# Performance work log

Hardware: AMD Instinct MI355X
Metric: run time of the kernel (lower is better)

## Reference

```python
import jax, jax.numpy as jnp
import numpy as np

B, L, H, V = 64, 2048, 256, 32000
BETA = 0.9
EPS_K = 1e-6   # delta-rule key-norm eps (matches torch 1e-06)
EPS_LN = 1e-5  # torch LayerNorm default eps


def setup_inputs() -> dict:
    key = jax.random.key(0)
    ks = jax.random.split(key, 8)
    s = lambda k, shape: (jax.random.normal(k, shape, jnp.float32) * 0.02)
    return {
        "seq": jax.random.randint(ks[0], (B, L), 0, V),
        "embed": s(ks[1], (V, H)),
        "W1": s(ks[2], (H, 2 * H)),
        "b1": jnp.zeros((2 * H,), jnp.float32),
        "W2": s(ks[3], (2 * H, H)),
        "b2": jnp.zeros((H,), jnp.float32),
        "gamma": jnp.ones((H,), jnp.float32),
        "beta_ln": jnp.zeros((H,), jnp.float32),
        "rp_W": s(ks[4], (H, H)),
        "rp_b": jnp.zeros((H,), jnp.float32),
        "out_W": s(ks[5], (H, V)),
        "out_b": jnp.zeros((V,), jnp.float32),
    }


def reference(seq, embed, W1, b1, W2, b2, gamma, beta_ln, rp_W, rp_b, out_W, out_b):
    # Encoder: embed -> FFN residual -> LayerNorm
    e = embed[seq]                                    # [B, L, H]
    ff = jnp.maximum(e @ W1 + b1, 0.0) @ W2 + b2      # [B, L, H]
    x = e + ff
    mu = jnp.mean(x, axis=-1, keepdims=True)
    var = jnp.mean((x - mu) ** 2, axis=-1, keepdims=True)
    h_all = (x - mu) / jnp.sqrt(var + EPS_LN) * gamma + beta_ln  # [B, L, H]

    # Momentum delta-rule fast-weight memory over first L-1 steps (k == v == h_t)
    ks_t = jnp.moveaxis(h_all[:, :-1, :], 1, 0)       # [L-1, B, H] time-major

    def step(M, k):
        vp = jnp.einsum('bij,bj->bi', M, k)            # predicted value
        d = k - vp / (jnp.sum(k * k, axis=-1, keepdims=True) + EPS_K)
        delta = d[:, :, None] * k[:, None, :]          # outer product [B, H, H]
        return BETA * M + (1.0 - BETA) * delta, None

    M0 = jnp.zeros((h_all.shape[0], H, H), h_all.dtype)
    M, _ = jax.lax.scan(step, M0, ks_t)

    # Readout with final token
    y = jnp.einsum('bij,bj->bi', M, h_all[:, -1, :])   # [B, H]
    return (y @ rp_W + rp_b) @ out_W + out_b           # [B, V]
```

## Files before the change

kernel.cpp:

```cpp
#include <hip/hip_runtime.h>


#define B_ 64
#define L_ 2048
#define H_ 256
#define V_ 32000

typedef unsigned short u16;
typedef __attribute__((ext_vector_type(8))) short bf16x8;
typedef __attribute__((ext_vector_type(16))) float f32x16;
typedef __attribute__((ext_vector_type(4))) float f32x4;

__device__ __forceinline__ float b2f(u16 u){ union{unsigned x; float f;} z; z.x = ((unsigned)u)<<16; return z.f; }
__device__ __forceinline__ u16 f2b(float f){ union{float f; unsigned x;} z; z.f = f; unsigned r = z.x + 0x7FFFu + ((z.x>>16)&1u); return (u16)(r>>16); }
__device__ __forceinline__ float san(float v){ return (v == v && v > -1e30f && v < 1e30f) ? v : 0.f; }

template<bool F32> __device__ __forceinline__ float ldw(const void* p, long i){
  if (F32) return ((const float*)p)[i];
  return b2f(((const u16*)p)[i]);
}
template<bool F32> __device__ __forceinline__ float4 ld4(const void* p, long i){
  if (F32) return *(const float4*)((const float*)p + i);
  ushort4 u = *(const ushort4*)((const u16*)p + i);
  return make_float4(b2f(u.x), b2f(u.y), b2f(u.z), b2f(u.w));
}

__device__ __forceinline__ int detect_f32(const void* embed){
  const u16* e = (const u16*)embed;
  unsigned v = e[2 * (threadIdx.x & 255)];
  int ex = (v >> 7) & 0xFF;
  int pl = (ex >= 0x66 && ex <= 0x7D) || ((v & 0x7FFFu) == 0u);
  int cnt = __syncthreads_count(pl);
  return cnt < 128;
}

__global__ __launch_bounds__(256) void sentinel_kernel(const void* embed, void* out, float val)
{
  int f32 = detect_f32(embed);
  long idx = (long)blockIdx.x * 256 + threadIdx.x;
  if (idx < (long)B_ * V_){
    if (f32) ((float*)out)[idx] = val;
    else     ((u16*)out)[idx]   = f2b(val);
  }
}

template<bool F32>
__device__ __forceinline__ void wprep_body(
    const void* __restrict__ W1, const void* __restrict__ W2,
    u16* __restrict__ w1f_hi, u16* __restrict__ w1f_lo,
    u16* __restrict__ w2f_hi, u16* __restrict__ w2f_lo)
{
  const int cid = blockIdx.x * 256 + threadIdx.x;
  const int lane = cid & 63;
  const int nl = lane & 31, kh = lane >> 5;
  if (cid < 16384){
    const int nt = cid >> 10, k16 = (cid >> 6) & 15;
    const int n = nt*32 + nl;
    const int k0 = k16*16 + kh*8;
    #pragma unroll
    for (int e = 0; e < 8; ++e){
      float v = ldw<F32>(W1, (long)(k0+e)*512 + n);
      unsigned bi = __float_as_uint(v);
      u16 hi = (u16)(bi >> 16);
      float hif = __uint_as_float(((unsigned)hi) << 16);
      w1f_hi[cid*8 + e] = hi;
      w1f_lo[cid*8 + e] = f2b(v - hif);
    }
  } else {
    const int c2 = cid - 16384;
    const int nt = c2 >> 11, k16 = (c2 >> 6) & 31;
    const int n = nt*32 + nl;
    const int k0 = k16*16 + kh*8;
    #pragma unroll
    for (int e = 0; e < 8; ++e){
      float v = ldw<F32>(W2, (long)(k0+e)*256 + n);
      unsigned bi = __float_as_uint(v);
      u16 hi = (u16)(bi >> 16);
      float hif = __uint_as_float(((unsigned)hi) << 16);
      w2f_hi[c2*8 + e] = hi;
      w2f_lo[c2*8 + e] = f2b(v - hif);
    }
  }
}

__global__ __launch_bounds__(256) void wprep_kernel(
    const void* __restrict__ embed,
    const void* __restrict__ W1, const void* __restrict__ W2,
    u16* __restrict__ wbuf)
{
  u16* w1h = wbuf;
  u16* w1l = wbuf + 131072;
  u16* w2h = wbuf + 262144;
  u16* w2l = wbuf + 393216;
  if (detect_f32(embed)) wprep_body<true >(W1, W2, w1h, w1l, w2h, w2l);
  else                   wprep_body<false>(W1, W2, w1h, w1l, w2h, w2l);
}

template<bool F32>
__device__ __forceinline__ void encm_body(
    u16* e_l, u16* t1_l, float* red, float* red2, float* stats,
    const int* __restrict__ seq, const void* __restrict__ embed,
    const u16* __restrict__ w1f_hi, const u16* __restrict__ w1f_lo,
    const u16* __restrict__ w2f_hi, const u16* __restrict__ w2f_lo,
    const void* __restrict__ b1, const void* __restrict__ b2,
    const void* __restrict__ gamma, const void* __restrict__ beta,
    u16* __restrict__ h)
{
  const int tid = threadIdx.x;
  const long tok0 = (long)blockIdx.x * 32;
  const int lane = tid & 63, wv = tid >> 6;
  const int col = lane & 31, hw = lane >> 5;

  {
    const int tr = tid >> 3, u0 = (tid & 7) * 4;
    int tk = seq[tok0 + tr];
    tk = (tk >= 0 && tk < V_) ? tk : 0;
    #pragma unroll
    for (int c = 0; c < 4; ++c){
      const int u = u0 + c;
      const int phys = u ^ (tr & 7);
      if (F32){
        const float4* sp = (const float4*)((const float*)embed + (long)tk*H_ + u*8);
        float4 v0 = sp[0], v1 = sp[1];
        ushort4 o0, o1;
        o0.x=f2b(v0.x); o0.y=f2b(v0.y); o0.z=f2b(v0.z); o0.w=f2b(v0.w);
        o1.x=f2b(v1.x); o1.y=f2b(v1.y); o1.z=f2b(v1.z); o1.w=f2b(v1.w);
        *(ushort4*)&e_l[tr*256 + phys*8]     = o0;
        *(ushort4*)&e_l[tr*256 + phys*8 + 4] = o1;
      } else {
        uint4 v = *(const uint4*)((const u16*)embed + (long)tk*H_ + u*8);
        *(uint4*)&e_l[tr*256 + phys*8] = v;
      }
    }
  }
  __syncthreads();

  {
    f32x16 acc[4];
    #pragma unroll
    for (int t = 0; t < 4; ++t)
      #pragma unroll
      for (int r = 0; r < 16; ++r) acc[t][r] = 0.f;

    #pragma unroll
    for (int k16 = 0; k16 < 16; ++k16){
      const int phys = (k16*2 + hw) ^ (col & 7);
      bf16x8 a = *(const bf16x8*)&e_l[col*256 + phys*8];
      #pragma unroll
      for (int t = 0; t < 4; ++t){
        const int off = (((wv*4 + t)*16 + k16)*64 + lane)*8;
        bf16x8 bh = *(const bf16x8*)&w1f_hi[off];
        bf16x8 bl = *(const bf16x8*)&w1f_lo[off];
        acc[t] = __builtin_amdgcn_mfma_f32_32x32x16_bf16(a, bh, acc[t], 0, 0, 0);
        acc[t] = __builtin_amdgcn_mfma_f32_32x32x16_bf16(a, bl, acc[t], 0, 0, 0);
      }
    }

    #pragma unroll
    for (int t = 0; t < 4; ++t){
      const int n = (wv*4 + t)*32 + col;
      const float bb = ldw<F32>(b1, n);
      const int u = n >> 3, nl = n & 7;
      #pragma unroll
      for (int r = 0; r < 16; ++r){
        const int m = (r&3) + 8*(r>>2) + 4*hw;
        float v = fmaxf(acc[t][r] + bb, 0.f);
        t1_l[m*512 + ((u ^ (m&7))<<3) + nl] = f2b(v);
      }
    }
  }
  __syncthreads();

  f32x16 acc2[2];
  #pragma unroll
  for (int t = 0; t < 2; ++t)
    #pragma unroll
    for (int r = 0; r < 16; ++r) acc2[t][r] = 0.f;

  #pragma unroll
  for (int k16 = 0; k16 < 32; ++k16){
    const int phys = (k16*2 + hw) ^ (col & 7);
    bf16x8 a = *(const bf16x8*)&t1_l[col*512 + phys*8];
    #pragma unroll
    for (int t = 0; t < 2; ++t){
      const int off = (((wv*2 + t)*32 + k16)*64 + lane)*8;
      bf16x8 bh = *(const bf16x8*)&w2f_hi[off];
      bf16x8 bl = *(const bf16x8*)&w2f_lo[off];
      acc2[t] = __builtin_amdgcn_mfma_f32_32x32x16_bf16(a, bh, acc2[t], 0, 0, 0);
      acc2[t] = __builtin_amdgcn_mfma_f32_32x32x16_bf16(a, bl, acc2[t], 0, 0, 0);
    }
  }
  __syncthreads();

  u16* xb = t1_l;
  #pragma unroll
  for (int t = 0; t < 2; ++t){
    const int n = (wv*2 + t)*32 + col;
    const float bb = ldw<F32>(b2, n);
    const int ue = n >> 3, nl = n & 7;
    #pragma unroll
    for (int r = 0; r < 16; ++r){
      const int m = (r&3) + 8*(r>>2) + 4*hw;
      float ev = b2f(e_l[m*256 + ((ue ^ (m&7))<<3) + nl]);
      float x = acc2[t][r] + bb + ev;
      xb[m*256 + n] = f2b(x);
    }
  }
  __syncthreads();

  {
    const int row = tid >> 3, seg = tid & 7;
    const u16* xr = &xb[row*256 + seg*32];
    float s = 0.f, q = 0.f;
    #pragma unroll
    for (int j = 0; j < 32; j += 4){
      ushort4 v4 = *(const ushort4*)&xr[j];
      float v0 = b2f(v4.x), v1 = b2f(v4.y), v2 = b2f(v4.z), v3 = b2f(v4.w);
      s += v0 + v1 + v2 + v3;
      q += v0*v0 + v1*v1 + v2*v2 + v3*v3;
    }
    red[row*8 + seg] = s;
    red2[row*8 + seg] = q;
  }
  __syncthreads();
  if (tid < 32){
    float s = 0.f, q = 0.f;
    #pragma unroll
    for (int j = 0; j < 8; ++j){ s += red[tid*8 + j]; q += red2[tid*8 + j]; }
    float mu = s * (1.f/256.f);
    float var = q * (1.f/256.f) - mu*mu;
    stats[tid] = mu;
    stats[32 + tid] = 1.f / sqrtf(fmaxf(var, 0.f) + 1e-5f);
  }
  __syncthreads();

  {
    const int row = tid >> 3, c0 = (tid & 7) * 32;
    const float mu = stats[row], rs = stats[32 + row];
    u16* hp = h + (tok0 + row)*H_ + c0;
    const u16* xr = &xb[row*256 + c0];
    #pragma unroll
    for (int j = 0; j < 32; j += 4){
      float4 g  = ld4<F32>(gamma, c0 + j);
      float4 be = ld4<F32>(beta,  c0 + j);
      ushort4 xv = *(const ushort4*)&xr[j];
      ushort4 o;
      o.x = f2b(san((b2f(xv.x) - mu)*rs*g.x + be.x));
      o.y = f2b(san((b2f(xv.y) - mu)*rs*g.y + be.y));
      o.z = f2b(san((b2f(xv.z) - mu)*rs*g.z + be.z));
      o.w = f2b(san((b2f(xv.w) - mu)*rs*g.w + be.w));
      *(ushort4*)&hp[j] = o;
    }
  }
}

__global__ __launch_bounds__(256) void encm_kernel(
    const int* __restrict__ seq, const void* __restrict__ embed,
    const u16* __restrict__ wbuf,
    const void* __restrict__ b1, const void* __restrict__ b2,
    const void* __restrict__ gamma, const void* __restrict__ beta,
    u16* __restrict__ h)
{
  __shared__ __align__(16) u16 e_l[32*256];
  __shared__ __align__(16) u16 t1_l[32*512];
  __shared__ float red[256];
  __shared__ float red2[256];
  __shared__ float stats[64];
  const u16* w1h = wbuf;
  const u16* w1l = wbuf + 131072;
  const u16* w2h = wbuf + 262144;
  const u16* w2l = wbuf + 393216;
  if (detect_f32(embed))
    encm_body<true >(e_l, t1_l, red, red2, stats, seq, embed, w1h, w1l, w2h, w2l, b1, b2, gamma, beta, h);
  else
    encm_body<false>(e_l, t1_l, red, red2, stats, seq, embed, w1h, w1l, w2h, w2l, b1, b2, gamma, beta, h);
}

template<bool F32>
__device__ __forceinline__ void enc_body(
    u16* sm,
    const int* __restrict__ seq, const void* __restrict__ embed,
    const void* __restrict__ W1, const void* __restrict__ b1,
    const void* __restrict__ W2, const void* __restrict__ b2,
    const void* __restrict__ gamma, const void* __restrict__ beta,
    u16* __restrict__ h)
{
  u16* eT  = sm;
  u16* t1T = sm + 8192;
  u16* xb  = sm + 24576;
  float* stats = (float*)sm;

  const int tid = threadIdx.x;
  const long tok0 = (long)blockIdx.x * 32;

  for (int idx = tid; idx < 8192; idx += 256){
    int r = idx >> 8, c = idx & 255;
    int tk = seq[tok0 + r];
    tk = (tk >= 0 && tk < V_) ? tk : 0;
    eT[c*32 + r] = f2b(ldw<F32>(embed, (long)tk*H_ + c));
  }
  __syncthreads();

  const int jg = tid & 31, rg = tid >> 5;
  const int r0 = rg * 4;

  for (int sl = 0; sl < 4; ++sl){
    const int j0 = sl*128 + jg*4;
    float acc[4][4] = {{0.f}};
    for (int c = 0; c < 256; ++c){
      ushort4 a4 = *(const ushort4*)&eT[c*32 + r0];
      float4 w = ld4<F32>(W1, (long)c*512 + j0);
      float a0=b2f(a4.x), a1=b2f(a4.y), a2=b2f(a4.z), a3=b2f(a4.w);
      acc[0][0]+=a0*w.x; acc[0][1]+=a0*w.y; acc[0][2]+=a0*w.z; acc[0][3]+=a0*w.w;
      acc[1][0]+=a1*w.x; acc[1][1]+=a1*w.y; acc[1][2]+=a1*w.z; acc[1][3]+=a1*w.w;
      acc[2][0]+=a2*w.x; acc[2][1]+=a2*w.y; acc[2][2]+=a2*w.z; acc[2][3]+=a2*w.w;
      acc[3][0]+=a3*w.x; acc[3][1]+=a3*w.y; acc[3][2]+=a3*w.z; acc[3][3]+=a3*w.w;
    }
    for (int jj = 0; jj < 4; ++jj){
      float bb = ldw<F32>(b1, j0+jj);
      ushort4 o;
      o.x = f2b(fmaxf(acc[0][jj]+bb, 0.f));
      o.y = f2b(fmaxf(acc[1][jj]+bb, 0.f));
      o.z = f2b(fmaxf(acc[2][jj]+bb, 0.f));
      o.w = f2b(fmaxf(acc[3][jj]+bb, 0.f));
      *(ushort4*)&t1T[(j0+jj)*32 + r0] = o;
    }
  }
  __syncthreads();

  for (int sl = 0; sl < 2; ++sl){
    const int co0 = sl*128 + jg*4;
    float acc[4][4] = {{0.f}};
    for (int c = 0; c < 512; ++c){
      ushort4 a4 = *(const ushort4*)&t1T[c*32 + r0];
      float4 w = ld4<F32>(W2, (long)c*256 + co0);
      float a0=b2f(a4.x), a1=b2f(a4.y), a2=b2f(a4.z), a3=b2f(a4.w);
      acc[0][0]+=a0*w.x; acc[0][1]+=a0*w.y; acc[0][2]+=a0*w.z; acc[0][3]+=a0*w.w;
      acc[1][0]+=a1*w.x; acc[1][1]+=a1*w.y; acc[1][2]+=a1*w.z; acc[1][3]+=a1*w.w;
      acc[2][0]+=a2*w.x; acc[2][1]+=a2*w.y; acc[2][2]+=a2*w.z; acc[2][3]+=a2*w.w;
      acc[3][0]+=a3*w.x; acc[3][1]+=a3*w.y; acc[3][2]+=a3*w.z; acc[3][3]+=a3*w.w;
    }
    float bb0 = ldw<F32>(b2, co0+0), bb1 = ldw<F32>(b2, co0+1);
    float bb2 = ldw<F32>(b2, co0+2), bb3 = ldw<F32>(b2, co0+3);
    for (int rr = 0; rr < 4; ++rr){
      float x0 = acc[rr][0] + bb0 + b2f(eT[(co0+0)*32 + r0+rr]);
      float x1 = acc[rr][1] + bb1 + b2f(eT[(co0+1)*32 + r0+rr]);
      float x2 = acc[rr][2] + bb2 + b2f(eT[(co0+2)*32 + r0+rr]);
      float x3 = acc[rr][3] + bb3 + b2f(eT[(co0+3)*32 + r0+rr]);
      ushort4 o; o.x=f2b(x0); o.y=f2b(x1); o.z=f2b(x2); o.w=f2b(x3);
      *(ushort4*)&xb[(r0+rr)*256 + co0] = o;
    }
  }
  __syncthreads();

  if (tid < 32){
    float s = 0.f, q = 0.f;
    for (int c = 0; c < 256; ++c){ float v = b2f(xb[tid*256 + c]); s += v; q += v*v; }
    float mu = s * (1.f/256.f);
    float var = q * (1.f/256.f) - mu*mu;
    stats[tid] = mu;
    stats[32 + tid] = 1.f / sqrtf(fmaxf(var, 0.f) + 1e-5f);
  }
  __syncthreads();
  for (int idx = tid; idx < 8192; idx += 256){
    int r = idx >> 8, c = idx & 255;
    float hv = (b2f(xb[idx]) - stats[r]) * stats[32+r] * ldw<F32>(gamma, c) + ldw<F32>(beta, c);
    h[(tok0 + r)*H_ + c] = f2b(san(hv));
  }
}

__global__ __launch_bounds__(256) void enc_kernel(
    const int* __restrict__ seq, const void* __restrict__ embed,
    const void* __restrict__ W1, const void* __restrict__ b1,
    const void* __restrict__ W2, const void* __restrict__ b2,
    const void* __restrict__ gamma, const void* __restrict__ beta,
    u16* __restrict__ h)
{
  __shared__ __align__(16) u16 sm[32768];
  if (detect_f32(embed)) enc_body<true >(sm, seq, embed, W1, b1, W2, b2, gamma, beta, h);
  else                   enc_body<false>(sm, seq, embed, W1, b1, W2, b2, gamma, beta, h);
}

__global__ __launch_bounds__(64) void winv_kernel(
    const u16* __restrict__ h, u16* __restrict__ w2g, float* __restrict__ scg)
{
  __shared__ __align__(16) u16 k_l[32*256];
  __shared__ float g_l[32*33];
  __shared__ float w_l[32*33];
  __shared__ float bp[33];

  const int tid = threadIdx.x;
  const int cb = blockIdx.x;
  const int b = cb >> 6, ch = cb & 63;
  const int col = tid & 31, hw = tid >> 5;
  const int C = (ch == 63) ? 31 : 32;

  if (tid < 33) bp[tid] = powf(0.9f, (float)tid);

  {
    const int t = tid >> 1, u0 = (tid & 1) * 16;
    const u16* src = h + ((long)b*L_ + ch*32 + t)*H_ + u0*8;
    #pragma unroll
    for (int c = 0; c < 16; ++c){
      uint4 v = make_uint4(0u,0u,0u,0u);
      if (t < C) v = *(const uint4*)(src + c*8);
      int phys = (u0 + c) ^ (t & 7);
      *(uint4*)&k_l[t*256 + phys*8] = v;
    }
  }
  __syncthreads();

  {
    f32x16 acc; for (int r = 0; r < 16; ++r) acc[r] = 0.f;
    #pragma unroll
    for (int s = 0; s < 16; ++s){
      int phys = (s*2 + hw) ^ (col & 7);
      bf16x8 a = *(const bf16x8*)&k_l[col*256 + phys*8];
      acc = __builtin_amdgcn_mfma_f32_32x32x16_bf16(a, a, acc, 0, 0, 0);
    }
    #pragma unroll
    for (int r = 0; r < 16; ++r){
      int row = (r&3) + 8*(r>>2) + 4*hw;
      g_l[row*33 + col] = acc[r];
    }
  }
  __syncthreads();

  if (tid < 32){
// ... 267 lines not shown
        int phys = ((j0 >> 3) + c) ^ (t & 7);
        *(uint4*)&k_l[t*256 + phys*8] = v;
      }
    }
    __syncthreads();

    if (wv == 1){
      f32x16 acc; for (int r=0;r<16;++r) acc[r]=0.f;
      #pragma unroll
      for (int s = 0; s < 16; ++s){
        int phys = (s*2 + hw) ^ (col & 7);
        bf16x8 a = *(const bf16x8*)&k_l[col*256 + phys*8];
        acc = __builtin_amdgcn_mfma_f32_32x32x16_bf16(a, a, acc, 0, 0, 0);
      }
      #pragma unroll
      for (int r = 0; r < 16; ++r){
        int row = (r&3) + 8*(r>>2) + 4*hw;
        g_l[row*33 + col] = acc[r];
      }
    } else {
      f32x16 acc; for (int r=0;r<16;++r) acc[r]=0.f;
      for (int s = 0; s < 16; ++s){
        int phys = (s*2 + hw) ^ (col & 7);
        bf16x8 a = *(const bf16x8*)&k_l[col*256 + phys*8];
        bf16x8 bh, bl;
        const float* mp = &M_l[col*257 + s*16 + hw*8];
        #pragma unroll
        for (int c = 0; c < 8; ++c){
          float f = mp[c];
          unsigned bi = __float_as_uint(f);
          bh[c] = (short)(bi >> 16);
          float hif = __uint_as_float(bi & 0xFFFF0000u);
          bl[c] = (short)f2b(f - hif);
        }
        acc = __builtin_amdgcn_mfma_f32_32x32x16_bf16(a, bh, acc, 0, 0, 0);
        acc = __builtin_amdgcn_mfma_f32_32x32x16_bf16(a, bl, acc, 0, 0, 0);
      }
      #pragma unroll
      for (int r = 0; r < 16; ++r){
        int row = (r&3) + 8*(r>>2) + 4*hw;
        d_l[row*33 + col] = acc[r];
      }
    }
    __syncthreads();

    #pragma unroll
    for (int p = 0; p < 8; ++p){
      int idx = p*128 + tid;
      int t = idx >> 5, i = idx & 31;
      float u = d_l[t*33 + i];
      int jg = ib*32 + i;
      float kti = b2f(k_l[t*256 + (((jg>>3) ^ (t&7))<<3) + (jg&7)]);
      float inv = 1.f / (g_l[t*33 + t] + 1e-6f);
      d_l[t*33 + i] = kti - bp[t] * u * inv;
    }
    __syncthreads();

    if (tid < 32){
      const int c = tid;
      for (int t = 1; t < C; ++t){
        float f = 0.1f / (g_l[t*33 + t] + 1e-6f);
        float acc = d_l[t*33 + c];
        for (int s = 0; s < t; ++s)
          acc -= f * bp[t-1-s] * g_l[t*33 + s] * d_l[s*33 + c];
        d_l[t*33 + c] = acc;
      }
    }
    __syncthreads();

    {
      const float bC = bp[C];
      bf16x8 bfr[2];
      #pragma unroll
      for (int h2 = 0; h2 < 2; ++h2){
        #pragma unroll
        for (int c = 0; c < 8; ++c){
          int t = h2*16 + hw*8 + c;
          int ci = C-1-t;
          float w = (ci >= 0) ? 0.1f * bp[ci] : 0.f;
          bfr[h2][c] = (short)f2b(d_l[t*33 + col] * w);
        }
      }
      for (int jt = wv*4; jt < wv*4 + 4; ++jt){
        f32x16 acc; for (int r=0;r<16;++r) acc[r]=0.f;
        #pragma unroll
        for (int h2 = 0; h2 < 2; ++h2){
          bf16x8 a;
          int j = jt*32 + col;
          #pragma unroll
          for (int c = 0; c < 8; ++c){
            int t = h2*16 + hw*8 + c;
            a[c] = (short)k_l[t*256 + (((j>>3) ^ (t&7))<<3) + (j&7)];
          }
          acc = __builtin_amdgcn_mfma_f32_32x32x16_bf16(a, bfr[h2], acc, 0, 0, 0);
        }
        #pragma unroll
        for (int r = 0; r < 16; ++r){
          int jrow = jt*32 + (r&3) + 8*(r>>2) + 4*hw;
          int addr = col*257 + jrow;
          M_l[addr] = bC * M_l[addr] + acc[r];
        }
      }
    }
    __syncthreads();
  }

  float* q_l = g_l;
  for (int p = tid; p < 256; p += 128) q_l[p] = b2f(hb[(long)(L_-1)*H_ + p]);
  __syncthreads();
  {
    int i = tid & 31, pt = tid >> 5;
    float s = 0.f;
    const float* mp = &M_l[i*257 + pt*64];
    const float* qp = &q_l[pt*64];
    for (int jj = 0; jj < 64; ++jj) s += mp[jj] * qp[jj];
    d_l[pt*33 + i] = s;
  }
  __syncthreads();
  if (tid < 32){
    float s = d_l[tid] + d_l[33 + tid] + d_l[66 + tid] + d_l[99 + tid];
    y[b*H_ + ib*32 + tid] = san(s);
  }
}

template<bool F32>
__device__ __forceinline__ void r1_body(
    float* yl, const float* __restrict__ y, const void* __restrict__ rpW,
    const void* __restrict__ rpb, float* __restrict__ zT)
{
  const int b = blockIdx.x, tid = threadIdx.x;
  yl[tid] = san(y[b*H_ + tid]);
  __syncthreads();
  float acc = ldw<F32>(rpb, tid);
  for (int j = 0; j < 256; ++j) acc += yl[j] * ldw<F32>(rpW, (long)j*H_ + tid);
  zT[tid*B_ + b] = san(acc);
}

__global__ __launch_bounds__(256) void r1_kernel(
    const void* __restrict__ embed, const float* __restrict__ y,
    const void* __restrict__ rpW, const void* __restrict__ rpb,
    float* __restrict__ zT)
{
  __shared__ float yl[256];
  if (detect_f32(embed)) r1_body<true >(yl, y, rpW, rpb, zT);
  else                   r1_body<false>(yl, y, rpW, rpb, zT);
}

template<bool F32>
__device__ __forceinline__ void r2_body(
    float* zl, const float* __restrict__ zT, const void* __restrict__ outW,
    const void* __restrict__ outb, void* __restrict__ out)
{
  const int tid = threadIdx.x;
  const int v = blockIdx.x*256 + tid;
  for (int idx = tid; idx < 16384; idx += 256) zl[idx] = zT[idx];
  __syncthreads();

  float ob = ldw<F32>(outb, v);
  float acc[64];
  #pragma unroll
  for (int bb = 0; bb < 64; ++bb) acc[bb] = ob;

  for (int i = 0; i < 256; ++i){
    float w = ldw<F32>(outW, (long)i*V_ + v);
    const float4* zp = (const float4*)&zl[i*64];
    #pragma unroll
    for (int q = 0; q < 16; ++q){
      float4 z4 = zp[q];
      acc[q*4+0] += w*z4.x; acc[q*4+1] += w*z4.y;
      acc[q*4+2] += w*z4.z; acc[q*4+3] += w*z4.w;
    }
  }
  if (F32){
    for (int bb = 0; bb < 64; ++bb) ((float*)out)[(long)bb*V_ + v] = san(acc[bb]);
  } else {
    for (int bb = 0; bb < 64; ++bb) ((u16*)out)[(long)bb*V_ + v] = f2b(san(acc[bb]));
  }
}

__global__ __launch_bounds__(256) void r2_kernel(
    const void* __restrict__ embed, const float* __restrict__ zT,
    const void* __restrict__ outW, const void* __restrict__ outb,
    void* __restrict__ out)
{
  __shared__ float zl[16384];
  if (detect_f32(embed)) r2_body<true >(zl, zT, outW, outb, out);
  else                   r2_body<false>(zl, zT, outW, outb, out);
}

extern "C" void kernel_launch(void* const* d_in, const int* in_sizes, int n_in,
                              void* d_out, int out_size, void* d_ws, size_t ws_size,
                              hipStream_t stream) {
  bool sizes_ok = (n_in == 12) && in_sizes
      && in_sizes[0] == B_*L_ && in_sizes[1] == V_*H_ && in_sizes[2] == H_*2*H_
      && in_sizes[3] == 2*H_  && in_sizes[4] == 2*H_*H_ && in_sizes[5] == H_
      && in_sizes[6] == H_    && in_sizes[7] == H_    && in_sizes[8] == H_*H_
      && in_sizes[9] == H_    && in_sizes[10] == H_*V_ && in_sizes[11] == V_;
  if (!sizes_ok){
    sentinel_kernel<<<(B_*V_ + 255)/256, 256, 0, stream>>>(d_in ? d_in[1] : d_out, d_out, 2000.0f);
    return;
  }
  if (ws_size < 67108864ull){
    sentinel_kernel<<<(B_*V_ + 255)/256, 256, 0, stream>>>(d_in[1], d_out, 1000.0f);
    return;
  }

  const int* seq   = (const int*)d_in[0];
  const void* embed= d_in[1];
  const void* W1   = d_in[2];
  const void* b1   = d_in[3];
  const void* W2   = d_in[4];
  const void* b2   = d_in[5];
  const void* gamma= d_in[6];
  const void* beta = d_in[7];
  const void* rpW  = d_in[8];
  const void* rpb  = d_in[9];
  const void* outW = d_in[10];
  const void* outb = d_in[11];

  u16*   h  = (u16*)d_ws;
  float* zT = (float*)d_ws;
  float* y  = (float*)d_out;

  const size_t need = 67108864ull + 8388608ull + 524288ull;
  if (ws_size >= need){
    u16*   wbuf = (u16*)  ((char*)d_ws + 67108864);
    u16*   w2g  = (u16*)  ((char*)d_ws + 67108864);
    float* scg  = (float*)((char*)d_ws + 67108864 + 8388608);
    wprep_kernel<<< 128, 256, 0, stream>>>(embed, W1, W2, wbuf);
    encm_kernel <<<4096, 256, 0, stream>>>(seq, embed, wbuf, b1, b2, gamma, beta, h);
    winv_kernel <<<4096,  64, 0, stream>>>(h, w2g, scg);
    scan_big    <<< 256, 512, 0, stream>>>(h, w2g, scg, y);
  } else {
    enc_kernel<<<4096, 256, 0, stream>>>(seq, embed, W1, b1, W2, b2, gamma, beta, h);
    scan_fallback<<<512, 128, 0, stream>>>(h, y);
  }

  r1_kernel<<< 64, 256, 0, stream>>>(embed, y, rpW, rpb, zT);
  r2_kernel<<<125, 256, 0, stream>>>(embed, zT, outW, outb, d_out);
}
```

Measured before the change: 686.4 us.

## Retile encoder to 64 tokens per 512-thread block and split readout over batch halves

```diff
diff --git a/kernel.cpp b/kernel.cpp
--- a/kernel.cpp
+++ b/kernel.cpp
@@ -107,7 +107,7 @@
     u16* __restrict__ h)
 {
   const int tid = threadIdx.x;
-  const long tok0 = (long)blockIdx.x * 32;
+  const long tok0 = (long)blockIdx.x * 64;
   const int lane = tid & 63, wv = tid >> 6;
   const int col = lane & 31, hw = lane >> 5;
 
@@ -135,42 +135,6 @@
   }
   __syncthreads();
 
-  {
-    f32x16 acc[4];
-    #pragma unroll
-    for (int t = 0; t < 4; ++t)
-      #pragma unroll
-      for (int r = 0; r < 16; ++r) acc[t][r] = 0.f;
-
-    #pragma unroll
-    for (int k16 = 0; k16 < 16; ++k16){
-      const int phys = (k16*2 + hw) ^ (col & 7);
-      bf16x8 a = *(const bf16x8*)&e_l[col*256 + phys*8];
-      #pragma unroll
-      for (int t = 0; t < 4; ++t){
-        const int off = (((wv*4 + t)*16 + k16)*64 + lane)*8;
-        bf16x8 bh = *(const bf16x8*)&w1f_hi[off];
-        bf16x8 bl = *(const bf16x8*)&w1f_lo[off];
-        acc[t] = __builtin_amdgcn_mfma_f32_32x32x16_bf16(a, bh, acc[t], 0, 0, 0);
-        acc[t] = __builtin_amdgcn_mfma_f32_32x32x16_bf16(a, bl, acc[t], 0, 0, 0);
-      }
-    }
-
-    #pragma unroll
-    for (int t = 0; t < 4; ++t){
-      const int n = (wv*4 + t)*32 + col;
-      const float bb = ldw<F32>(b1, n);
-      const int u = n >> 3, nl = n & 7;
-      #pragma unroll
-      for (int r = 0; r < 16; ++r){
-        const int m = (r&3) + 8*(r>>2) + 4*hw;
-        float v = fmaxf(acc[t][r] + bb, 0.f);
-        t1_l[m*512 + ((u ^ (m&7))<<3) + nl] = f2b(v);
-      }
-    }
-  }
-  __syncthreads();
-
   f32x16 acc2[2];
   #pragma unroll
   for (int t = 0; t < 2; ++t)
@@ -178,32 +142,73 @@
     for (int r = 0; r < 16; ++r) acc2[t][r] = 0.f;
 
   #pragma unroll
-  for (int k16 = 0; k16 < 32; ++k16){
-    const int phys = (k16*2 + hw) ^ (col & 7);
-    bf16x8 a = *(const bf16x8*)&t1_l[col*512 + phys*8];
-    #pragma unroll
-    for (int t = 0; t < 2; ++t){
-      const int off = (((wv*2 + t)*32 + k16)*64 + lane)*8;
+  for (int ss = 0; ss < 2; ++ss){
+    {
+      f32x16 acc1[2];
+      #pragma unroll
+      for (int t = 0; t < 2; ++t)
+        #pragma unroll
+        for (int r = 0; r < 16; ++r) acc1[t][r] = 0.f;
+
+      const int ntg = ss*8 + wv;
+      #pragma unroll
+      for (int k16 = 0; k16 < 16; ++k16){
+        const int phys = (k16*2 + hw) ^ (col & 7);
+        bf16x8 a0 = *(const bf16x8*)&e_l[col*256 + phys*8];
+        bf16x8 a1 = *(const bf16x8*)&e_l[(col+32)*256 + phys*8];
+        const int off = ((ntg*16 + k16)*64 + lane)*8;
+        bf16x8 bh = *(const bf16x8*)&w1f_hi[off];
+        bf16x8 bl = *(const bf16x8*)&w1f_lo[off];
+        acc1[0] = __builtin_amdgcn_mfma_f32_32x32x16_bf16(a0, bh, acc1[0], 0, 0, 0);
+        acc1[0] = __builtin_amdgcn_mfma_f32_32x32x16_bf16(a0, bl, acc1[0], 0, 0, 0);
+        acc1[1] = __builtin_amdgcn_mfma_f32_32x32x16_bf16(a1, bh, acc1[1], 0, 0, 0);
+        acc1[1] = __builtin_amdgcn_mfma_f32_32x32x16_bf16(a1, bl, acc1[1], 0, 0, 0);
+      }
+      const int n = wv*32 + col;
+      const float bb = ldw<F32>(b1, ntg*32 + col);
+      const int u = n >> 3, nl = n & 7;
+      #pragma unroll
+      for (int mt = 0; mt < 2; ++mt){
+        #pragma unroll
+        for (int r = 0; r < 16; ++r){
+          const int m = mt*32 + (r&3) + 8*(r>>2) + 4*hw;
+          float v = fmaxf(acc1[mt][r] + bb, 0.f);
+          t1_l[m*256 + ((u ^ (m&7))<<3) + nl] = f2b(v);
+        }
+      }
+    }
+    __syncthreads();
+
+    #pragma unroll
+    for (int k16 = 0; k16 < 16; ++k16){
+      const int phys = (k16*2 + hw) ^ (col & 7);
+      bf16x8 a0 = *(const bf16x8*)&t1_l[col*256 + phys*8];
+      bf16x8 a1 = *(const bf16x8*)&t1_l[(col+32)*256 + phys*8];
+      const int off = ((wv*32 + ss*16 + k16)*64 + lane)*8;
       bf16x8 bh = *(const bf16x8*)&w2f_hi[off];
       bf16x8 bl = *(const bf16x8*)&w2f_lo[off];
-      acc2[t] = __builtin_amdgcn_mfma_f32_32x32x16_bf16(a, bh, acc2[t], 0, 0, 0);
-      acc2[t] = __builtin_amdgcn_mfma_f32_32x32x16_bf16(a, bl, acc2[t], 0, 0, 0);
-    }
-  }
-  __syncthreads();
+      acc2[0] = __builtin_amdgcn_mfma_f32_32x32x16_bf16(a0, bh, acc2[0], 0, 0, 0);
+      acc2[0] = __builtin_amdgcn_mfma_f32_32x32x16_bf16(a0, bl, acc2[0], 0, 0, 0);
+      acc2[1] = __builtin_amdgcn_mfma_f32_32x32x16_bf16(a1, bh, acc2[1], 0, 0, 0);
+      acc2[1] = __builtin_amdgcn_mfma_f32_32x32x16_bf16(a1, bl, acc2[1], 0, 0, 0);
+    }
+    __syncthreads();
+  }
 
   u16* xb = t1_l;
-  #pragma unroll
-  for (int t = 0; t < 2; ++t){
-    const int n = (wv*2 + t)*32 + col;
+  {
+    const int n = wv*32 + col;
     const float bb = ldw<F32>(b2, n);
     const int ue = n >> 3, nl = n & 7;
     #pragma unroll
-    for (int r = 0; r < 16; ++r){
-      const int m = (r&3) + 8*(r>>2) + 4*hw;
-      float ev = b2f(e_l[m*256 + ((ue ^ (m&7))<<3) + nl]);
-      float x = acc2[t][r] + bb + ev;
-      xb[m*256 + n] = f2b(x);
+    for (int mt = 0; mt < 2; ++mt){
+      #pragma unroll
+      for (int r = 0; r < 16; ++r){
+        const int m = mt*32 + (r&3) + 8*(r>>2) + 4*hw;
+        float ev = b2f(e_l[m*256 + ((ue ^ (m&7))<<3) + nl]);
+        float x = acc2[mt][r] + bb + ev;
+        xb[m*256 + n] = f2b(x);
+      }
     }
   }
   __syncthreads();
@@ -223,20 +228,20 @@
     red2[row*8 + seg] = q;
   }
   __syncthreads();
-  if (tid < 32){
+  if (tid < 64){
     float s = 0.f, q = 0.f;
     #pragma unroll
     for (int j = 0; j < 8; ++j){ s += red[tid*8 + j]; q += red2[tid*8 + j]; }
     float mu = s * (1.f/256.f);
     float var = q * (1.f/256.f) - mu*mu;
     stats[tid] = mu;
-    stats[32 + tid] = 1.f / sqrtf(fmaxf(var, 0.f) + 1e-5f);
+    stats[64 + tid] = 1.f / sqrtf(fmaxf(var, 0.f) + 1e-5f);
   }
   __syncthreads();
 
   {
     const int row = tid >> 3, c0 = (tid & 7) * 32;
-    const float mu = stats[row], rs = stats[32 + row];
+    const float mu = stats[row], rs = stats[64 + row];
     u16* hp = h + (tok0 + row)*H_ + c0;
     const u16* xr = &xb[row*256 + c0];
     #pragma unroll
@@ -254,18 +259,18 @@
   }
 }
 
-__global__ __launch_bounds__(256) void encm_kernel(
+__global__ __launch_bounds__(512, 4) void encm_kernel(
     const int* __restrict__ seq, const void* __restrict__ embed,
     const u16* __restrict__ wbuf,
     const void* __restrict__ b1, const void* __restrict__ b2,
     const void* __restrict__ gamma, const void* __restrict__ beta,
     u16* __restrict__ h)
 {
-  __shared__ __align__(16) u16 e_l[32*256];
-  __shared__ __align__(16) u16 t1_l[32*512];
-  __shared__ float red[256];
-  __shared__ float red2[256];
-  __shared__ float stats[64];
+  __shared__ __align__(16) u16 e_l[64*256];
+  __shared__ __align__(16) u16 t1_l[64*256];
+  __shared__ float red[512];
+  __shared__ float red2[512];
+  __shared__ float stats[128];
   const u16* w1h = wbuf;
   const u16* w1l = wbuf + 131072;
   const u16* w2h = wbuf + 262144;
@@ -847,29 +852,33 @@
     const void* __restrict__ outb, void* __restrict__ out)
 {
   const int tid = threadIdx.x;
-  const int v = blockIdx.x*256 + tid;
-  for (int idx = tid; idx < 16384; idx += 256) zl[idx] = zT[idx];
+  const int half = blockIdx.x / 125;
+  const int v = (blockIdx.x % 125)*256 + tid;
+  for (int idx = tid; idx < 8192; idx += 256){
+    int i = idx >> 5, bb = idx & 31;
+    zl[idx] = zT[i*64 + half*32 + bb];
+  }
   __syncthreads();
 
   float ob = ldw<F32>(outb, v);
-  float acc[64];
+  float acc[32];
   #pragma unroll
-  for (int bb = 0; bb < 64; ++bb) acc[bb] = ob;
+  for (int bb = 0; bb < 32; ++bb) acc[bb] = ob;
 
   for (int i = 0; i < 256; ++i){
     float w = ldw<F32>(outW, (long)i*V_ + v);
-    const float4* zp = (const float4*)&zl[i*64];
-    #pragma unroll
-    for (int q = 0; q < 16; ++q){
+    const float4* zp = (const float4*)&zl[i*32];
+    #pragma unroll
+    for (int q = 0; q < 8; ++q){
       float4 z4 = zp[q];
       acc[q*4+0] += w*z4.x; acc[q*4+1] += w*z4.y;
       acc[q*4+2] += w*z4.z; acc[q*4+3] += w*z4.w;
     }
   }
   if (F32){
-    for (int bb = 0; bb < 64; ++bb) ((float*)out)[(long)bb*V_ + v] = san(acc[bb]);
+    for (int bb = 0; bb < 32; ++bb) ((float*)out)[(long)(half*32 + bb)*V_ + v] = san(acc[bb]);
   } else {
-    for (int bb = 0; bb < 64; ++bb) ((u16*)out)[(long)bb*V_ + v] = f2b(san(acc[bb]));
+    for (int bb = 0; bb < 32; ++bb) ((u16*)out)[(long)(half*32 + bb)*V_ + v] = f2b(san(acc[bb]));
   }
 }
 
@@ -878,7 +887,7 @@
     const void* __restrict__ outW, const void* __restrict__ outb,
     void* __restrict__ out)
 {
-  __shared__ float zl[16384];
+  __shared__ float zl[8192];
   if (detect_f32(embed)) r2_body<true >(zl, zT, outW, outb, out);
   else                   r2_body<false>(zl, zT, outW, outb, out);
 }
@@ -923,7 +932,7 @@
     u16*   w2g  = (u16*)  ((char*)d_ws + 67108864);
     float* scg  = (float*)((char*)d_ws + 67108864 + 8388608);
     wprep_kernel<<< 128, 256, 0, stream>>>(embed, W1, W2, wbuf);
-    encm_kernel <<<4096, 256, 0, stream>>>(seq, embed, wbuf, b1, b2, gamma, beta, h);
+    encm_kernel <<<2048, 512, 0, stream>>>(seq, embed, wbuf, b1, b2, gamma, beta, h);
     winv_kernel <<<4096,  64, 0, stream>>>(h, w2g, scg);
     scan_big    <<< 256, 512, 0, stream>>>(h, w2g, scg, y);
   } else {
@@ -932,5 +941,5 @@
   }
 
   r1_kernel<<< 64, 256, 0, stream>>>(embed, y, rpW, rpb, zT);
-  r2_kernel<<<125, 256, 0, stream>>>(embed, zT, outW, outb, d_out);
-}
+  r2_kernel<<<250, 256, 0, stream>>>(embed, zT, outW, outb, d_out);
+}
```

After: 759.4 us. 1.11x slower.

## Chunk encoder FFN hidden dim to halve LDS and split readout batch across blocks

Applied to the files above, without the earlier changes.

```diff
diff --git a/kernel.cpp b/kernel.cpp
--- a/kernel.cpp
+++ b/kernel.cpp
@@ -98,7 +98,7 @@
 
 template<bool F32>
 __device__ __forceinline__ void encm_body(
-    u16* e_l, u16* t1_l, float* red, float* red2, float* stats,
+    u16* e_l, u16* t1s, float* red, float* red2, float* stats,
     const int* __restrict__ seq, const void* __restrict__ embed,
     const u16* __restrict__ w1f_hi, const u16* __restrict__ w1f_lo,
     const u16* __restrict__ w2f_hi, const u16* __restrict__ w2f_lo,
@@ -135,42 +135,6 @@
   }
   __syncthreads();
 
-  {
-    f32x16 acc[4];
-    #pragma unroll
-    for (int t = 0; t < 4; ++t)
-      #pragma unroll
-      for (int r = 0; r < 16; ++r) acc[t][r] = 0.f;
-
-    #pragma unroll
-    for (int k16 = 0; k16 < 16; ++k16){
-      const int phys = (k16*2 + hw) ^ (col & 7);
-      bf16x8 a = *(const bf16x8*)&e_l[col*256 + phys*8];
-      #pragma unroll
-      for (int t = 0; t < 4; ++t){
-        const int off = (((wv*4 + t)*16 + k16)*64 + lane)*8;
-        bf16x8 bh = *(const bf16x8*)&w1f_hi[off];
-        bf16x8 bl = *(const bf16x8*)&w1f_lo[off];
-        acc[t] = __builtin_amdgcn_mfma_f32_32x32x16_bf16(a, bh, acc[t], 0, 0, 0);
-        acc[t] = __builtin_amdgcn_mfma_f32_32x32x16_bf16(a, bl, acc[t], 0, 0, 0);
-      }
-    }
-
-    #pragma unroll
-    for (int t = 0; t < 4; ++t){
-      const int n = (wv*4 + t)*32 + col;
-      const float bb = ldw<F32>(b1, n);
-      const int u = n >> 3, nl = n & 7;
-      #pragma unroll
-      for (int r = 0; r < 16; ++r){
-        const int m = (r&3) + 8*(r>>2) + 4*hw;
-        float v = fmaxf(acc[t][r] + bb, 0.f);
-        t1_l[m*512 + ((u ^ (m&7))<<3) + nl] = f2b(v);
-      }
-    }
-  }
-  __syncthreads();
-
   f32x16 acc2[2];
   #pragma unroll
   for (int t = 0; t < 2; ++t)
@@ -178,30 +142,69 @@
     for (int r = 0; r < 16; ++r) acc2[t][r] = 0.f;
 
   #pragma unroll
-  for (int k16 = 0; k16 < 32; ++k16){
-    const int phys = (k16*2 + hw) ^ (col & 7);
-    bf16x8 a = *(const bf16x8*)&t1_l[col*512 + phys*8];
-    #pragma unroll
-    for (int t = 0; t < 2; ++t){
-      const int off = (((wv*2 + t)*32 + k16)*64 + lane)*8;
-      bf16x8 bh = *(const bf16x8*)&w2f_hi[off];
-      bf16x8 bl = *(const bf16x8*)&w2f_lo[off];
-      acc2[t] = __builtin_amdgcn_mfma_f32_32x32x16_bf16(a, bh, acc2[t], 0, 0, 0);
-      acc2[t] = __builtin_amdgcn_mfma_f32_32x32x16_bf16(a, bl, acc2[t], 0, 0, 0);
-    }
-  }
-  __syncthreads();
-
-  u16* xb = t1_l;
+  for (int ss = 0; ss < 2; ++ss){
+    {
+      f32x16 acc1[2];
+      #pragma unroll
+      for (int t = 0; t < 2; ++t)
+        #pragma unroll
+        for (int r = 0; r < 16; ++r) acc1[t][r] = 0.f;
+
+      #pragma unroll
+      for (int k16 = 0; k16 < 16; ++k16){
+        const int phys = (k16*2 + hw) ^ (col & 7);
+        bf16x8 a = *(const bf16x8*)&e_l[col*256 + phys*8];
+        #pragma unroll
+        for (int t = 0; t < 2; ++t){
+          const int ntg = ss*8 + wv*2 + t;
+          const int off = ((ntg*16 + k16)*64 + lane)*8;
+          bf16x8 bh = *(const bf16x8*)&w1f_hi[off];
+          bf16x8 bl = *(const bf16x8*)&w1f_lo[off];
+          acc1[t] = __builtin_amdgcn_mfma_f32_32x32x16_bf16(a, bh, acc1[t], 0, 0, 0);
+          acc1[t] = __builtin_amdgcn_mfma_f32_32x32x16_bf16(a, bl, acc1[t], 0, 0, 0);
+        }
+      }
+      #pragma unroll
+      for (int t = 0; t < 2; ++t){
+        const int nl = (wv*2 + t)*32 + col;
+        const float bb = ldw<F32>(b1, (ss*8 + wv*2 + t)*32 + col);
+        const int u = nl >> 3, nlo = nl & 7;
+        #pragma unroll
+        for (int r = 0; r < 16; ++r){
+          const int m = (r&3) + 8*(r>>2) + 4*hw;
+          float v = fmaxf(acc1[t][r] + bb, 0.f);
+          t1s[m*256 + ((u ^ (m&7))<<3) + nlo] = f2b(v);
+        }
+      }
+    }
+    __syncthreads();
+
+    #pragma unroll
+    for (int k16 = 0; k16 < 16; ++k16){
+      const int phys = (k16*2 + hw) ^ (col & 7);
+      bf16x8 a = *(const bf16x8*)&t1s[col*256 + phys*8];
+      #pragma unroll
+      for (int t = 0; t < 2; ++t){
+        const int off = (((wv*2 + t)*32 + ss*16 + k16)*64 + lane)*8;
+        bf16x8 bh = *(const bf16x8*)&w2f_hi[off];
+        bf16x8 bl = *(const bf16x8*)&w2f_lo[off];
+        acc2[t] = __builtin_amdgcn_mfma_f32_32x32x16_bf16(a, bh, acc2[t], 0, 0, 0);
+        acc2[t] = __builtin_amdgcn_mfma_f32_32x32x16_bf16(a, bl, acc2[t], 0, 0, 0);
+      }
+    }
+    __syncthreads();
+  }
+
+  u16* xb = t1s;
   #pragma unroll
   for (int t = 0; t < 2; ++t){
     const int n = (wv*2 + t)*32 + col;
     const float bb = ldw<F32>(b2, n);
-    const int ue = n >> 3, nl = n & 7;
+    const int ue = n >> 3, nlo = n & 7;
     #pragma unroll
     for (int r = 0; r < 16; ++r){
       const int m = (r&3) + 8*(r>>2) + 4*hw;
-      float ev = b2f(e_l[m*256 + ((ue ^ (m&7))<<3) + nl]);
+      float ev = b2f(e_l[m*256 + ((ue ^ (m&7))<<3) + nlo]);
       float x = acc2[t][r] + bb + ev;
       xb[m*256 + n] = f2b(x);
     }
@@ -262,7 +265,7 @@
     u16* __restrict__ h)
 {
   __shared__ __align__(16) u16 e_l[32*256];
-  __shared__ __align__(16) u16 t1_l[32*512];
+  __shared__ __align__(16) u16 t1s[32*256];
   __shared__ float red[256];
   __shared__ float red2[256];
   __shared__ float stats[64];
@@ -271,9 +274,9 @@
   const u16* w2h = wbuf + 262144;
   const u16* w2l = wbuf + 393216;
   if (detect_f32(embed))
-    encm_body<true >(e_l, t1_l, red, red2, stats, seq, embed, w1h, w1l, w2h, w2l, b1, b2, gamma, beta, h);
+    encm_body<true >(e_l, t1s, red, red2, stats, seq, embed, w1h, w1l, w2h, w2l, b1, b2, gamma, beta, h);
   else
-    encm_body<false>(e_l, t1_l, red, red2, stats, seq, embed, w1h, w1l, w2h, w2l, b1, b2, gamma, beta, h);
+    encm_body<false>(e_l, t1s, red, red2, stats, seq, embed, w1h, w1l, w2h, w2l, b1, b2, gamma, beta, h);
 }
 
 template<bool F32>
@@ -847,29 +850,33 @@
     const void* __restrict__ outb, void* __restrict__ out)
 {
   const int tid = threadIdx.x;
-  const int v = blockIdx.x*256 + tid;
-  for (int idx = tid; idx < 16384; idx += 256) zl[idx] = zT[idx];
+  const int half = blockIdx.x / 125;
+  const int v = (blockIdx.x % 125)*256 + tid;
+  for (int idx = tid; idx < 8192; idx += 256){
+    int i = idx >> 5, bb = idx & 31;
+    zl[idx] = zT[i*64 + half*32 + bb];
+  }
   __syncthreads();
 
   float ob = ldw<F32>(outb, v);
-  float acc[64];
+  float acc[32];
   #pragma unroll
-  for (int bb = 0; bb < 64; ++bb) acc[bb] = ob;
+  for (int bb = 0; bb < 32; ++bb) acc[bb] = ob;
 
   for (int i = 0; i < 256; ++i){
     float w = ldw<F32>(outW, (long)i*V_ + v);
-    const float4* zp = (const float4*)&zl[i*64];
-    #pragma unroll
-    for (int q = 0; q < 16; ++q){
+    const float4* zp = (const float4*)&zl[i*32];
+    #pragma unroll
+    for (int q = 0; q < 8; ++q){
       float4 z4 = zp[q];
       acc[q*4+0] += w*z4.x; acc[q*4+1] += w*z4.y;
       acc[q*4+2] += w*z4.z; acc[q*4+3] += w*z4.w;
     }
   }
   if (F32){
-    for (int bb = 0; bb < 64; ++bb) ((float*)out)[(long)bb*V_ + v] = san(acc[bb]);
+    for (int bb = 0; bb < 32; ++bb) ((float*)out)[(long)(half*32 + bb)*V_ + v] = san(acc[bb]);
   } else {
-    for (int bb = 0; bb < 64; ++bb) ((u16*)out)[(long)bb*V_ + v] = f2b(san(acc[bb]));
+    for (int bb = 0; bb < 32; ++bb) ((u16*)out)[(long)(half*32 + bb)*V_ + v] = f2b(san(acc[bb]));
   }
 }
 
@@ -878,7 +885,7 @@
     const void* __restrict__ outW, const void* __restrict__ outb,
     void* __restrict__ out)
 {
-  __shared__ float zl[16384];
+  __shared__ float zl[8192];
   if (detect_f32(embed)) r2_body<true >(zl, zT, outW, outb, out);
   else                   r2_body<false>(zl, zT, outW, outb, out);
 }
@@ -932,5 +939,5 @@
   }
 
   r1_kernel<<< 64, 256, 0, stream>>>(embed, y, rpW, rpb, zT);
-  r2_kernel<<<125, 256, 0, stream>>>(embed, zT, outW, outb, d_out);
-}
+  r2_kernel<<<250, 256, 0, stream>>>(embed, zT, outW, outb, d_out);
+}
```

Measured after the change: 826.0 us. 1.2x slower.

## Switch encoder GEMMs to 16x16x32 MFMA tiles with 512-thread blocks

Applied to the files above, without the earlier changes.

```diff
diff --git a/kernel.cpp b/kernel.cpp
--- a/kernel.cpp
+++ b/kernel.cpp
@@ -52,11 +52,11 @@
 {
   const int cid = blockIdx.x * 256 + threadIdx.x;
   const int lane = cid & 63;
-  const int nl = lane & 31, kh = lane >> 5;
+  const int nl = lane & 15, kh = lane >> 4;
   if (cid < 16384){
-    const int nt = cid >> 10, k16 = (cid >> 6) & 15;
-    const int n = nt*32 + nl;
-    const int k0 = k16*16 + kh*8;
+    const int n16 = cid >> 9, k32 = (cid >> 6) & 7;
+    const int n = n16*16 + nl;
+    const int k0 = k32*32 + kh*8;
     #pragma unroll
     for (int e = 0; e < 8; ++e){
       float v = ldw<F32>(W1, (long)(k0+e)*512 + n);
@@ -68,9 +68,9 @@
     }
   } else {
     const int c2 = cid - 16384;
-    const int nt = c2 >> 11, k16 = (c2 >> 6) & 31;
-    const int n = nt*32 + nl;
-    const int k0 = k16*16 + kh*8;
+    const int n16 = c2 >> 10, k32 = (c2 >> 6) & 15;
+    const int n = n16*16 + nl;
+    const int k0 = k32*32 + kh*8;
     #pragma unroll
     for (int e = 0; e < 8; ++e){
       float v = ldw<F32>(W2, (long)(k0+e)*256 + n);
@@ -109,14 +109,15 @@
   const int tid = threadIdx.x;
   const long tok0 = (long)blockIdx.x * 32;
   const int lane = tid & 63, wv = tid >> 6;
-  const int col = lane & 31, hw = lane >> 5;
+  const int li = lane & 15, kg = lane >> 4;
+  const int lx = li & 7;
 
   {
-    const int tr = tid >> 3, u0 = (tid & 7) * 4;
+    const int tr = tid >> 4, u0 = (tid & 15) * 2;
     int tk = seq[tok0 + tr];
     tk = (tk >= 0 && tk < V_) ? tk : 0;
     #pragma unroll
-    for (int c = 0; c < 4; ++c){
+    for (int c = 0; c < 2; ++c){
       const int u = u0 + c;
       const int phys = u ^ (tr & 7);
       if (F32){
@@ -135,73 +136,91 @@
   }
   __syncthreads();
 
-  {
-    f32x16 acc[4];
-    #pragma unroll
-    for (int t = 0; t < 4; ++t)
-      #pragma unroll
-      for (int r = 0; r < 16; ++r) acc[t][r] = 0.f;
-
-    #pragma unroll
-    for (int k16 = 0; k16 < 16; ++k16){
-      const int phys = (k16*2 + hw) ^ (col & 7);
-      bf16x8 a = *(const bf16x8*)&e_l[col*256 + phys*8];
-      #pragma unroll
-      for (int t = 0; t < 4; ++t){
-        const int off = (((wv*4 + t)*16 + k16)*64 + lane)*8;
-        bf16x8 bh = *(const bf16x8*)&w1f_hi[off];
-        bf16x8 bl = *(const bf16x8*)&w1f_lo[off];
-        acc[t] = __builtin_amdgcn_mfma_f32_32x32x16_bf16(a, bh, acc[t], 0, 0, 0);
-        acc[t] = __builtin_amdgcn_mfma_f32_32x32x16_bf16(a, bl, acc[t], 0, 0, 0);
-      }
-    }
-
+  #pragma unroll
+  for (int g = 0; g < 2; ++g){
+    f32x4 acc[4];
     #pragma unroll
     for (int t = 0; t < 4; ++t){
-      const int n = (wv*4 + t)*32 + col;
+      acc[t][0]=0.f; acc[t][1]=0.f; acc[t][2]=0.f; acc[t][3]=0.f;
+    }
+    const int nA = wv*4 + g*2, nB = nA + 1;
+    #pragma unroll
+    for (int k32 = 0; k32 < 8; ++k32){
+      const int u = k32*4 + kg;
+      bf16x8 a0 = *(const bf16x8*)&e_l[li*256 + ((u ^ lx)<<3)];
+      bf16x8 a1 = *(const bf16x8*)&e_l[(li+16)*256 + ((u ^ lx)<<3)];
+      const int offA = ((nA*8 + k32)*64 + lane)*8;
+      const int offB = ((nB*8 + k32)*64 + lane)*8;
+      bf16x8 bhA = *(const bf16x8*)&w1f_hi[offA];
+      bf16x8 blA = *(const bf16x8*)&w1f_lo[offA];
+      bf16x8 bhB = *(const bf16x8*)&w1f_hi[offB];
+      bf16x8 blB = *(const bf16x8*)&w1f_lo[offB];
+      acc[0] = __builtin_amdgcn_mfma_f32_16x16x32_bf16(a0, bhA, acc[0], 0, 0, 0);
+      acc[1] = __builtin_amdgcn_mfma_f32_16x16x32_bf16(a1, bhA, acc[1], 0, 0, 0);
+      acc[2] = __builtin_amdgcn_mfma_f32_16x16x32_bf16(a0, bhB, acc[2], 0, 0, 0);
+      acc[3] = __builtin_amdgcn_mfma_f32_16x16x32_bf16(a1, bhB, acc[3], 0, 0, 0);
+      acc[0] = __builtin_amdgcn_mfma_f32_16x16x32_bf16(a0, blA, acc[0], 0, 0, 0);
+      acc[1] = __builtin_amdgcn_mfma_f32_16x16x32_bf16(a1, blA, acc[1], 0, 0, 0);
+      acc[2] = __builtin_amdgcn_mfma_f32_16x16x32_bf16(a0, blB, acc[2], 0, 0, 0);
+      acc[3] = __builtin_amdgcn_mfma_f32_16x16x32_bf16(a1, blB, acc[3], 0, 0, 0);
+    }
+    #pragma unroll
+    for (int t = 0; t < 4; ++t){
+      const int m16 = t & 1;
+      const int n16 = (t >> 1) ? nB : nA;
+      const int n = n16*16 + li;
       const float bb = ldw<F32>(b1, n);
-      const int u = n >> 3, nl = n & 7;
-      #pragma unroll
-      for (int r = 0; r < 16; ++r){
-        const int m = (r&3) + 8*(r>>2) + 4*hw;
+      const int un = n >> 3, no = n & 7;
+      #pragma unroll
+      for (int r = 0; r < 4; ++r){
+        const int m = m16*16 + kg*4 + r;
         float v = fmaxf(acc[t][r] + bb, 0.f);
-        t1_l[m*512 + ((u ^ (m&7))<<3) + nl] = f2b(v);
-      }
-    }
-  }
-  __syncthreads();
-
-  f32x16 acc2[2];
+        t1_l[m*512 + ((un ^ (m&7))<<3) + no] = f2b(v);
+      }
+    }
+  }
+  __syncthreads();
+
+  f32x4 acc2[4];
   #pragma unroll
-  for (int t = 0; t < 2; ++t)
-    #pragma unroll
-    for (int r = 0; r < 16; ++r) acc2[t][r] = 0.f;
-
+  for (int t = 0; t < 4; ++t){
+    acc2[t][0]=0.f; acc2[t][1]=0.f; acc2[t][2]=0.f; acc2[t][3]=0.f;
+  }
+  const int nA2 = wv*2, nB2 = wv*2 + 1;
   #pragma unroll
-  for (int k16 = 0; k16 < 32; ++k16){
-    const int phys = (k16*2 + hw) ^ (col & 7);
-    bf16x8 a = *(const bf16x8*)&t1_l[col*512 + phys*8];
-    #pragma unroll
-    for (int t = 0; t < 2; ++t){
-      const int off = (((wv*2 + t)*32 + k16)*64 + lane)*8;
-      bf16x8 bh = *(const bf16x8*)&w2f_hi[off];
-      bf16x8 bl = *(const bf16x8*)&w2f_lo[off];
-      acc2[t] = __builtin_amdgcn_mfma_f32_32x32x16_bf16(a, bh, acc2[t], 0, 0, 0);
-      acc2[t] = __builtin_amdgcn_mfma_f32_32x32x16_bf16(a, bl, acc2[t], 0, 0, 0);
-    }
+  for (int k32 = 0; k32 < 16; ++k32){
+    const int u = k32*4 + kg;
+    bf16x8 a0 = *(const bf16x8*)&t1_l[li*512 + ((u ^ lx)<<3)];
+    bf16x8 a1 = *(const bf16x8*)&t1_l[(li+16)*512 + ((u ^ lx)<<3)];
+    const int offA = ((nA2*16 + k32)*64 + lane)*8;
+    const int offB = ((nB2*16 + k32)*64 + lane)*8;
+    bf16x8 bhA = *(const bf16x8*)&w2f_hi[offA];
+    bf16x8 blA = *(const bf16x8*)&w2f_lo[offA];
+    bf16x8 bhB = *(const bf16x8*)&w2f_hi[offB];
+    bf16x8 blB = *(const bf16x8*)&w2f_lo[offB];
+    acc2[0] = __builtin_amdgcn_mfma_f32_16x16x32_bf16(a0, bhA, acc2[0], 0, 0, 0);
+    acc2[1] = __builtin_amdgcn_mfma_f32_16x16x32_bf16(a1, bhA, acc2[1], 0, 0, 0);
+    acc2[2] = __builtin_amdgcn_mfma_f32_16x16x32_bf16(a0, bhB, acc2[2], 0, 0, 0);
+    acc2[3] = __builtin_amdgcn_mfma_f32_16x16x32_bf16(a1, bhB, acc2[3], 0, 0, 0);
+    acc2[0] = __builtin_amdgcn_mfma_f32_16x16x32_bf16(a0, blA, acc2[0], 0, 0, 0);
+    acc2[1] = __builtin_amdgcn_mfma_f32_16x16x32_bf16(a1, blA, acc2[1], 0, 0, 0);
+    acc2[2] = __builtin_amdgcn_mfma_f32_16x16x32_bf16(a0, blB, acc2[2], 0, 0, 0);
+    acc2[3] = __builtin_amdgcn_mfma_f32_16x16x32_bf16(a1, blB, acc2[3], 0, 0, 0);
   }
   __syncthreads();
 
   u16* xb = t1_l;
   #pragma unroll
-  for (int t = 0; t < 2; ++t){
-    const int n = (wv*2 + t)*32 + col;
+  for (int t = 0; t < 4; ++t){
+    const int m16 = t & 1;
+    const int n16 = (t >> 1) ? nB2 : nA2;
+    const int n = n16*16 + li;
     const float bb = ldw<F32>(b2, n);
-    const int ue = n >> 3, nl = n & 7;
-    #pragma unroll
-    for (int r = 0; r < 16; ++r){
-      const int m = (r&3) + 8*(r>>2) + 4*hw;
-      float ev = b2f(e_l[m*256 + ((ue ^ (m&7))<<3) + nl]);
+    const int ue = n >> 3, no = n & 7;
+    #pragma unroll
+    for (int r = 0; r < 4; ++r){
+      const int m = m16*16 + kg*4 + r;
+      float ev = b2f(e_l[m*256 + ((ue ^ (m&7))<<3) + no]);
       float x = acc2[t][r] + bb + ev;
       xb[m*256 + n] = f2b(x);
     }
@@ -209,24 +228,24 @@
   __syncthreads();
 
   {
-    const int row = tid >> 3, seg = tid & 7;
-    const u16* xr = &xb[row*256 + seg*32];
+    const int row = tid >> 4, seg = tid & 15;
+    const u16* xr = &xb[row*256 + seg*16];
     float s = 0.f, q = 0.f;
     #pragma unroll
-    for (int j = 0; j < 32; j += 4){
+    for (int j = 0; j < 16; j += 4){
       ushort4 v4 = *(const ushort4*)&xr[j];
       float v0 = b2f(v4.x), v1 = b2f(v4.y), v2 = b2f(v4.z), v3 = b2f(v4.w);
       s += v0 + v1 + v2 + v3;
       q += v0*v0 + v1*v1 + v2*v2 + v3*v3;
     }
-    red[row*8 + seg] = s;
-    red2[row*8 + seg] = q;
+    red[row*16 + seg] = s;
+    red2[row*16 + seg] = q;
   }
   __syncthreads();
   if (tid < 32){
     float s = 0.f, q = 0.f;
     #pragma unroll
-    for (int j = 0; j < 8; ++j){ s += red[tid*8 + j]; q += red2[tid*8 + j]; }
+    for (int j = 0; j < 16; ++j){ s += red[tid*16 + j]; q += red2[tid*16 + j]; }
     float mu = s * (1.f/256.f);
     float var = q * (1.f/256.f) - mu*mu;
     stats[tid] = mu;
@@ -235,12 +254,12 @@
   __syncthreads();
 
   {
-    const int row = tid >> 3, c0 = (tid & 7) * 32;
+    const int row = tid >> 4, c0 = (tid & 15) * 16;
     const float mu = stats[row], rs = stats[32 + row];
     u16* hp = h + (tok0 + row)*H_ + c0;
     const u16* xr = &xb[row*256 + c0];
     #pragma unroll
-    for (int j = 0; j < 32; j += 4){
+    for (int j = 0; j < 16; j += 4){
       float4 g  = ld4<F32>(gamma, c0 + j);
       float4 be = ld4<F32>(beta,  c0 + j);
       ushort4 xv = *(const ushort4*)&xr[j];
@@ -254,7 +273,7 @@
   }
 }
 
-__global__ __launch_bounds__(256) void encm_kernel(
+__global__ __launch_bounds__(512, 4) void encm_kernel(
     const int* __restrict__ seq, const void* __restrict__ embed,
     const u16* __restrict__ wbuf,
     const void* __restrict__ b1, const void* __restrict__ b2,
@@ -263,8 +282,8 @@
 {
   __shared__ __align__(16) u16 e_l[32*256];
   __shared__ __align__(16) u16 t1_l[32*512];
-  __shared__ float red[256];
-  __shared__ float red2[256];
+  __shared__ float red[512];
+  __shared__ float red2[512];
   __shared__ float stats[64];
   const u16* w1h = wbuf;
   const u16* w1l = wbuf + 131072;
@@ -923,7 +942,7 @@
     u16*   w2g  = (u16*)  ((char*)d_ws + 67108864);
     float* scg  = (float*)((char*)d_ws + 67108864 + 8388608);
     wprep_kernel<<< 128, 256, 0, stream>>>(embed, W1, W2, wbuf);
-    encm_kernel <<<4096, 256, 0, stream>>>(seq, embed, wbuf, b1, b2, gamma, beta, h);
+    encm_kernel <<<4096, 512, 0, stream>>>(seq, embed, wbuf, b1, b2, gamma, beta, h);
     winv_kernel <<<4096,  64, 0, stream>>>(h, w2g, scg);
     scan_big    <<< 256, 512, 0, stream>>>(h, w2g, scg, y);
   } else {
```

New measurement: 672.4 us. -2.0%, faster.
